# Kernel optimization log

Hardware: AMD Instinct MI355X
Metric: run time of the kernel (lower is better)

## Reference

```python
import jax, jax.numpy as jnp
import numpy as np

N, E, F_IN, H1, H2, C = 100000, 800000, 182, 128, 64, 2


def setup_inputs() -> dict:
    key = jax.random.key(0)
    ks = jax.random.split(key, 10)
    s = 0.05
    return {
        "x": jax.random.normal(ks[0], (N, F_IN), dtype=jnp.float32),
        "edge_index": jax.random.randint(ks[1], (2, E), 0, N, dtype=jnp.int32),
        "W1_l": jax.random.normal(ks[2], (H1, F_IN), dtype=jnp.float32) * s,
        "W1_r": jax.random.normal(ks[3], (H1, F_IN), dtype=jnp.float32) * s,
        "b1": jnp.zeros((H1,), dtype=jnp.float32),
        "W2_l": jax.random.normal(ks[4], (H2, H1), dtype=jnp.float32) * s,
        "W2_r": jax.random.normal(ks[5], (H2, H1), dtype=jnp.float32) * s,
        "b2": jnp.zeros((H2,), dtype=jnp.float32),
        "W_lin": jax.random.normal(ks[6], (C, H2), dtype=jnp.float32) * s,
        "b_lin": jnp.zeros((C,), dtype=jnp.float32),
    }


def _sage_conv(x, src, dst, Wl, Wr, b):
    # mean-aggregate neighbor messages x[src] onto dst, then two linears
    msg = x[src]                                            # [E, F]
    ssum = jax.ops.segment_sum(msg, dst, num_segments=N)    # [N, F]
    cnt = jax.ops.segment_sum(jnp.ones((src.shape[0], 1), x.dtype), dst, num_segments=N)
    mean = ssum / jnp.maximum(cnt, 1.0)                     # [N, F]
    return mean @ Wl.T + x @ Wr.T + b                       # [N, F_out]


def reference(x, edge_index, W1_l, W1_r, b1, W2_l, W2_r, b2, W_lin, b_lin):
    src, dst = edge_index[0], edge_index[1]
    h = jax.nn.relu(_sage_conv(x, src, dst, W1_l, W1_r, b1))   # dropout is identity in eval
    h = jax.nn.relu(_sage_conv(h, src, dst, W2_l, W2_r, b2))
    logits = h @ W_lin.T + b_lin
    return jax.nn.log_softmax(logits, axis=1)
```

## Files before the change

### kernel.cpp

```cpp
#include <hip/hip_runtime.h>
#include <hip/hip_bf16.h>
#include <math.h>

#define F_IN 182
#define H1   128
#define H2   64

typedef short bf16x8 __attribute__((ext_vector_type(8)));
typedef float f32x4 __attribute__((ext_vector_type(4)));

__device__ __forceinline__ float b2f(short s) {
    unsigned u = ((unsigned)(unsigned short)s) << 16;
    return __builtin_bit_cast(float, u);
}
__device__ __forceinline__ short f2b(float f) {
    return __builtin_bit_cast(short, __float2bfloat16(f));
}
__device__ __forceinline__ short2 f2x2(float2 f) {
    short2 r;
    r.x = f2b(f.x);
    r.y = f2b(f.y);
    return r;
}

#define GLOAD16(g, l) __builtin_amdgcn_global_load_lds( \
    (const __attribute__((address_space(1))) void*)(g), \
    (__attribute__((address_space(3))) void*)(l), 16, 0, 0)

__global__ __launch_bounds__(256) void prelude(
    int* __restrict__ cnt, int Nn, int zB,
    const float* __restrict__ W1l, const float* __restrict__ W1r, short* __restrict__ wc1,
    const float* __restrict__ W2l, const float* __restrict__ W2r, short* __restrict__ wc2)
{
    int b = blockIdx.x, tid = threadIdx.x;
    if (b < zB) {
        int i = (b * 256 + tid) * 4;
        if (i + 4 <= Nn) {
            int4 z = make_int4(0, 0, 0, 0);
            *(int4*)(cnt + i) = z;
        } else {
            for (int j = i; j < Nn; ++j) cnt[j] = 0;
        }
        return;
    }
    b -= zB;
    if (b < 192) {
        int idx = b * 256 + tid;
        int r = idx / 192, k = idx - r * 192;
        float v = 0.f;
        if (k < F_IN) v = (r < 128) ? W1l[r * F_IN + k] : W1r[(r - 128) * F_IN + k];
        wc1[idx] = f2b(v);
        return;
    }
    b -= 192;
    {
        int idx = b * 256 + tid;
        int r = idx >> 7, k = idx & 127;
        float v = (r < 64) ? W2l[r * 128 + k] : W2r[(r - 64) * 128 + k];
        wc2[idx] = f2b(v);
    }
}

__global__ __launch_bounds__(256) void scan_block(const int* __restrict__ in,
                                                  int* __restrict__ out,
                                                  int* __restrict__ bsums, int Nn) {
    __shared__ int s[256];
    int b = blockIdx.x, t = threadIdx.x;
    int base = b * 2048 + t * 8;
    int v[8]; int sum = 0;
#pragma unroll
    for (int i = 0; i < 8; ++i) { int idx = base + i; v[i] = (idx < Nn) ? in[idx] : 0; sum += v[i]; }
    s[t] = sum; __syncthreads();
    for (int off = 1; off < 256; off <<= 1) {
        int x = (t >= off) ? s[t - off] : 0; __syncthreads();
        s[t] += x; __syncthreads();
    }
    int excl = s[t] - sum;
    if (t == 255) bsums[b] = s[255];
    int run = excl;
#pragma unroll
    for (int i = 0; i < 8; ++i) { int idx = base + i; if (idx < Nn) out[idx] = run; run += v[i]; }
}

__global__ __launch_bounds__(256) void scan_add(int* __restrict__ offs,
                                                const int* __restrict__ bsums,
                                                int nb, int Nn) {
    __shared__ int sbs[64];
    int t = threadIdx.x;
    if (t < 64) {
        int v = (t < nb) ? bsums[t] : 0;
        int s = v;
#pragma unroll
        for (int off = 1; off < 64; off <<= 1) {
            int u = __shfl_up(s, off, 64);
            if (t >= off) s += u;
        }
        sbs[t] = s - v;
    }
    __syncthreads();
    int i = blockIdx.x * 256 + t;
    if (i < Nn) offs[i] += sbs[i >> 11];
}

__global__ __launch_bounds__(256) void csr_scatter(const int* __restrict__ srcv,
                                                   const int* __restrict__ dstv,
                                                   const int* __restrict__ rank,
                                                   const int* __restrict__ offs,
                                                   int* __restrict__ csr, int E) {
    int base = (blockIdx.x * 256 + threadIdx.x) * 8;
    if (base + 8 <= E) {
        int4 d0 = *(const int4*)(dstv + base);
        int4 d1 = *(const int4*)(dstv + base + 4);
        int4 s0 = *(const int4*)(srcv + base);
        int4 s1 = *(const int4*)(srcv + base + 4);
        int4 r0 = *(const int4*)(rank + base);
        int4 r1 = *(const int4*)(rank + base + 4);
        csr[offs[d0.x] + r0.x] = s0.x;
        csr[offs[d0.y] + r0.y] = s0.y;
        csr[offs[d0.z] + r0.z] = s0.z;
        csr[offs[d0.w] + r0.w] = s0.w;
        csr[offs[d1.x] + r1.x] = s1.x;
        csr[offs[d1.y] + r1.y] = s1.y;
        csr[offs[d1.z] + r1.z] = s1.z;
        csr[offs[d1.w] + r1.w] = s1.w;
    } else {
        for (int e = base; e < E; ++e) csr[offs[dstv[e]] + rank[e]] = srcv[e];
    }
}

template <int NC, int KK, int KREAL, bool DEG>
__global__ __launch_bounds__(512) void gemm_fused(
    const void* __restrict__ Ap, const short* __restrict__ Wcat,
    short* __restrict__ outL, short* __restrict__ outR, int M,
    const int* __restrict__ dstv, int* __restrict__ cnt, int* __restrict__ rank,
    int E, int degB)
{
    constexpr int BM = 128, BK = 64;
    constexpr int WN = NC / 4;
    constexpr int NJ = WN / 16;
    constexpr int CB = NC * 8 / 512;
    __shared__ __attribute__((aligned(16))) short sA[BM * BK];
    __shared__ __attribute__((aligned(16))) short sB[NC * BK];
    int tid = threadIdx.x;

    if (DEG && (int)blockIdx.x < degB) {
        int tstep = degB * 512 * 4;
        int gtid = (int)blockIdx.x * 512 + tid;
        for (int base = gtid * 4; base + 4 <= E; base += tstep) {
            int4 d = *(const int4*)(dstv + base);
            int4 rk;
            rk.x = atomicAdd(&cnt[d.x], 1);
            rk.y = atomicAdd(&cnt[d.y], 1);
            rk.z = atomicAdd(&cnt[d.z], 1);
            rk.w = atomicAdd(&cnt[d.w], 1);
            *(int4*)(rank + base) = rk;
        }
        if (gtid == 0) {
            for (int e = E & ~3; e < E; ++e) rank[e] = atomicAdd(&cnt[dstv[e]], 1);
        }
        return;
    }
    int bx = DEG ? ((int)blockIdx.x - degB) : (int)blockIdx.x;
    int wid = tid >> 6, lane = tid & 63;
    int wr = wid >> 2, wc = wid & 3;
    int row0 = bx * BM;
    f32x4 acc[4][NJ] = {};
#pragma unroll
    for (int ksi = 0; ksi < KK / BK; ++ksi) {
        const int k0 = ksi * BK;
        {
            const float* Af = (const float*)Ap;
#pragma unroll
            for (int it = 0; it < 2; ++it) {
                int i = it * 512 + tid;
                int r = i >> 3, oct = i & 7;
                int gr = row0 + r;
                int gk = k0 + oct * 8;
                bf16x8 v = {};
                if (gr < M) {
                    const float* p = Af + (size_t)gr * KREAL + gk;
                    if (k0 + BK <= KREAL) {
                        float2 f0 = *(const float2*)(p + 0);
                        float2 f1 = *(const float2*)(p + 2);
                        float2 f2 = *(const float2*)(p + 4);
                        float2 f3 = *(const float2*)(p + 6);
                        short2 p0 = f2x2(f0), p1 = f2x2(f1), p2 = f2x2(f2), p3 = f2x2(f3);
                        v[0] = p0.x; v[1] = p0.y; v[2] = p1.x; v[3] = p1.y;
                        v[4] = p2.x; v[5] = p2.y; v[6] = p3.x; v[7] = p3.y;
                    } else {
#pragma unroll
                        for (int j = 0; j < 4; ++j) {
                            if (gk + 2 * j + 2 <= KREAL) {
                                short2 pj = f2x2(*(const float2*)(p + 2 * j));
                                v[2 * j] = pj.x; v[2 * j + 1] = pj.y;
                            }
                        }
                    }
                }
                *(bf16x8*)((char*)sA + r * 128 + ((oct * 16) ^ ((r & 7) << 4))) = v;
            }
        }
#pragma unroll
        for (int c = 0; c < CB; ++c) {
            int idx = (wid * CB + c) * 64 + lane;
            int r = idx >> 3, cs = (idx & 7) * 16;
            const char* g = (const char*)Wcat + (size_t)r * (KK * 2) + k0 * 2 + (cs ^ ((r & 7) << 4));
            GLOAD16(g, (char*)sB + (size_t)(wid * CB + c) * 1024);
        }
        __syncthreads();
        int rl = lane & 15;
        int sw = (rl & 7) << 4;
#pragma unroll
        for (int ks = 0; ks < 2; ++ks) {
            int kb2 = ks * 64 + (lane >> 4) * 16;
            int cswz = kb2 ^ sw;
            bf16x8 af[4];
#pragma unroll
            for (int mi = 0; mi < 4; ++mi) {
                int row = wr * 64 + mi * 16 + rl;
                af[mi] = *(const bf16x8*)((const char*)sA + row * 128 + cswz);
            }
#pragma unroll
            for (int ni = 0; ni < NJ; ++ni) {
                int rowb = wc * WN + ni * 16 + rl;
                bf16x8 bfr = *(const bf16x8*)((const char*)sB + rowb * 128 + cswz);
#pragma unroll
                for (int mi = 0; mi < 4; ++mi)
                    acc[mi][ni] = __builtin_amdgcn_mfma_f32_16x16x32_bf16(af[mi], bfr, acc[mi][ni], 0, 0, 0);
            }
        }
        __syncthreads();
    }
    constexpr int HN = NC / 2;
#pragma unroll
    for (int mi = 0; mi < 4; ++mi) {
#pragma unroll
        for (int ni = 0; ni < NJ; ++ni) {
            int gc = wc * WN + ni * 16 + (lane & 15);
#pragma unroll
            for (int r = 0; r < 4; ++r) {
                int gr = row0 + wr * 64 + mi * 16 + (lane >> 4) * 4 + r;
                if (gr < M) {
                    short v = f2b(acc[mi][ni][r]);
                    if (gc < HN) outL[(size_t)gr * HN + gc] = v;
                    else         outR[(size_t)gr * HN + gc - HN] = v;
                }
            }
        }
    }
}

__global__ __launch_bounds__(512) void agg_gemm2(
    const int* __restrict__ offs, const int* __restrict__ degs, const int* __restrict__ csr,
    const short* __restrict__ y1l, const short* __restrict__ y1r,
    const float* __restrict__ b1, const short* __restrict__ wc2,
    short* __restrict__ outL, short* __restrict__ outR, int M)
{
    constexpr int BM = 128, NC = 128;
    constexpr int WN = NC / 4;
    constexpr int NJ = WN / 16;
    __shared__ __attribute__((aligned(16))) short sA[BM * 128];
    __shared__ __attribute__((aligned(16))) short sB[NC * 128];
    int tid = threadIdx.x;
    int wid = tid >> 6, lane = tid & 63;
    int wr = wid >> 2, wc = wid & 3;
    int row0 = (int)blockIdx.x * BM;

#pragma unroll
    for (int it = 0; it < 4; ++it) {
        int idx = (wid * 4 + it) * 64 + lane;
        int r = idx >> 4, c16 = (idx & 15) * 16;
        const char* g = (const char*)wc2 + (size_t)r * 256 + (c16 ^ ((r & 7) << 4));
        GLOAD16(g, (char*)sB + (size_t)(wid * 4 + it) * 1024);
    }

    int rlocal = tid >> 4;
    int l = tid & 15;
    const int co = l * 8;
#pragma unroll
    for (int rr = 0; rr < 4; ++rr) {
        int r = rr * 32 + rlocal;
        int gid = row0 + r;
        bf16x8 o = {};
        if (gid < M) {
            int start = offs[gid], deg = degs[gid];
            float a[8] = {};
            int t = 0;
            for (; t + 8 <= deg; t += 8) {
                int idx[8];
#pragma unroll
                for (int q = 0; q < 8; ++q) idx[q] = csr[start + t + q];
                bf16x8 vv[8];
#pragma unroll
                for (int q = 0; q < 8; ++q) vv[q] = *(const bf16x8*)(y1l + (size_t)idx[q] * H1 + co);
#pragma unroll
                for (int j = 0; j < 8; ++j) {
                    float s = 0.f;
#pragma unroll
                    for (int q = 0; q < 8; ++q) s += b2f(vv[q][j]);
                    a[j] += s;
                }
            }
            for (; t + 4 <= deg; t += 4) {
                int i0 = csr[start + t], i1 = csr[start + t + 1];
                int i2 = csr[start + t + 2], i3 = csr[start + t + 3];
                bf16x8 v0 = *(const bf16x8*)(y1l + (size_t)i0 * H1 + co);
                bf16x8 v1 = *(const bf16x8*)(y1l + (size_t)i1 * H1 + co);
                bf16x8 v2 = *(const bf16x8*)(y1l + (size_t)i2 * H1 + co);
                bf16x8 v3 = *(const bf16x8*)(y1l + (size_t)i3 * H1 + co);
#pragma unroll
                for (int j = 0; j < 8; ++j)
                    a[j] += b2f(v0[j]) + b2f(v1[j]) + b2f(v2[j]) + b2f(v3[j]);
            }
            for (; t < deg; ++t) {
                int s = csr[start + t];
                bf16x8 v = *(const bf16x8*)(y1l + (size_t)s * H1 + co);
#pragma unroll
                for (int j = 0; j < 8; ++j) a[j] += b2f(v[j]);
            }
            float inv = 1.f / fmaxf((float)deg, 1.f);
            bf16x8 rv = *(const bf16x8*)(y1r + (size_t)gid * H1 + co);
#pragma unroll
            for (int j = 0; j < 8; ++j)
                o[j] = f2b(fmaxf(a[j] * inv + b2f(rv[j]) + b1[co + j], 0.f));
        }
        *(bf16x8*)((char*)sA + r * 256 + ((co * 2) ^ ((r & 7) << 4))) = o;
    }
    __syncthreads();

    f32x4 acc[4][NJ] = {};
    int rl = lane & 15;
    int sw = (rl & 7) << 4;
#pragma unroll
    for (int ks = 0; ks < 4; ++ks) {
        int kcol = (ks * 4 + (lane >> 4)) * 16;
        int cswz = kcol ^ sw;
        bf16x8 af[4];
#pragma unroll
        for (int mi = 0; mi < 4; ++mi) {
            int row = wr * 64 + mi * 16 + rl;
            af[mi] = *(const bf16x8*)((const char*)sA + row * 256 + cswz);
        }
#pragma unroll
        for (int ni = 0; ni < NJ; ++ni) {
            int rowb = wc * WN + ni * 16 + rl;
            bf16x8 bfr = *(const bf16x8*)((const char*)sB + rowb * 256 + cswz);
#pragma unroll
            for (int mi = 0; mi < 4; ++mi)
                acc[mi][ni] = __builtin_amdgcn_mfma_f32_16x16x32_bf16(af[mi], bfr, acc[mi][ni], 0, 0, 0);
        }
    }
    constexpr int HN = NC / 2;
#pragma unroll
    for (int mi = 0; mi < 4; ++mi) {
#pragma unroll
        for (int ni = 0; ni < NJ; ++ni) {
            int gc = wc * WN + ni * 16 + (lane & 15);
#pragma unroll
            for (int r = 0; r < 4; ++r) {
                int gr = row0 + wr * 64 + mi * 16 + (lane >> 4) * 4 + r;
                if (gr < M) {
                    short v = f2b(acc[mi][ni][r]);
                    if (gc < HN) outL[(size_t)gr * HN + gc] = v;
                    else         outR[(size_t)gr * HN + gc - HN] = v;
                }
            }
        }
    }
}

__global__ __launch_bounds__(256) void agg_head2(const int* __restrict__ offs,
                                                 const int* __restrict__ degs,
                                                 const int* __restrict__ csr,
                                                 const short* __restrict__ yl,
                                                 const short* __restrict__ yr,
                                                 const float* __restrict__ bias,
                                                 const float* __restrict__ Wlin,
                                                 const float* __restrict__ blin,
                                                 float* __restrict__ out, int Nn) {
    int gid = blockIdx.x * 16 + (threadIdx.x >> 4);
    int l = threadIdx.x & 15;
    if (gid >= Nn) return;
    int start = offs[gid], deg = degs[gid];
    const int co = l * 4;
    float a[4] = {};
    int t = 0;
    for (; t + 8 <= deg; t += 8) {
        int idx[8];
#pragma unroll
        for (int q = 0; q < 8; ++q) idx[q] = csr[start + t + q];
        short4 vv[8];
#pragma unroll
        for (int q = 0; q < 8; ++q) vv[q] = *(const short4*)(yl + (size_t)idx[q] * H2 + co);
#pragma unroll
        for (int q = 0; q < 8; ++q) {
            a[0] += b2f(vv[q].x); a[1] += b2f(vv[q].y);
            a[2] += b2f(vv[q].z); a[3] += b2f(vv[q].w);
        }
    }
    for (; t + 4 <= deg; t += 4) {
        int i0 = csr[start + t], i1 = csr[start + t + 1];
        int i2 = csr[start + t + 2], i3 = csr[start + t + 3];
        short4 v0 = *(const short4*)(yl + (size_t)i0 * H2 + co);
        short4 v1 = *(const short4*)(yl + (size_t)i1 * H2 + co);
        short4 v2 = *(const short4*)(yl + (size_t)i2 * H2 + co);
        short4 v3 = *(const short4*)(yl + (size_t)i3 * H2 + co);
        a[0] += b2f(v0.x) + b2f(v1.x) + b2f(v2.x) + b2f(v3.x);
        a[1] += b2f(v0.y) + b2f(v1.y) + b2f(v2.y) + b2f(v3.y);
        a[2] += b2f(v0.z) + b2f(v1.z) + b2f(v2.z) + b2f(v3.z);
        a[3] += b2f(v0.w) + b2f(v1.w) + b2f(v2.w) + b2f(v3.w);
    }
    for (; t < deg; ++t) {
        int s = csr[start + t];
        short4 v = *(const short4*)(yl + (size_t)s * H2 + co);
        a[0] += b2f(v.x); a[1] += b2f(v.y); a[2] += b2f(v.z); a[3] += b2f(v.w);
    }
    float inv = 1.f / fmaxf((float)deg, 1.f);
    short4 rv = *(const short4*)(yr + (size_t)gid * H2 + co);
    float h0 = fmaxf(a[0] * inv + b2f(rv.x) + bias[co + 0], 0.f);
    float h1v = fmaxf(a[1] * inv + b2f(rv.y) + bias[co + 1], 0.f);
    float h2v = fmaxf(a[2] * inv + b2f(rv.z) + bias[co + 2], 0.f);
    float h3v = fmaxf(a[3] * inv + b2f(rv.w) + bias[co + 3], 0.f);
    float g0 = h0 * Wlin[co] + h1v * Wlin[co + 1] + h2v * Wlin[co + 2] + h3v * Wlin[co + 3];
    float g1 = h0 * Wlin[64 + co] + h1v * Wlin[64 + co + 1] + h2v * Wlin[64 + co + 2] + h3v * Wlin[64 + co + 3];
#pragma unroll
    for (int m = 8; m >= 1; m >>= 1) {
        g0 += __shfl_xor(g0, m, 16);
        g1 += __shfl_xor(g1, m, 16);
    }
    if (l == 0) {
        g0 += blin[0]; g1 += blin[1];
        float mx = fmaxf(g0, g1);
        float lse = mx + logf(expf(g0 - mx) + expf(g1 - mx));
        float2 r; r.x = g0 - lse; r.y = g1 - lse;
        ((float2*)out)[gid] = r;
    }
}

extern "C" void kernel_launch(void* const* d_in, const int* in_sizes, int n_in,
                              void* d_out, int out_size, void* d_ws, size_t ws_size,
                              hipStream_t stream) {
    const float* x    = (const float*)d_in[0];
    const int*   ei   = (const int*)d_in[1];
    const float* W1l  = (const float*)d_in[2];
    const float* W1r  = (const float*)d_in[3];
    const float* b1   = (const float*)d_in[4];
    const float* W2l  = (const float*)d_in[5];
    const float* W2r  = (const float*)d_in[6];
    const float* b2   = (const float*)d_in[7];
    const float* Wlin = (const float*)d_in[8];
    const float* blin = (const float*)d_in[9];
    float* outp = (float*)d_out;

    const int N = in_sizes[0] / F_IN;
    const int E = in_sizes[1] / 2;
    const int* srcv = ei;
    const int* dstv = ei + E;

    char* ws = (char*)d_ws;
    size_t o = 0;
    auto alloc = [&](size_t bytes) { size_t r = o; o += (bytes + 255) & ~(size_t)255; return r; };
    int* cnt_i  = (int*)(ws + alloc((size_t)N * 4));
    int* offs   = (int*)(ws + alloc((size_t)N * 4));
    int* bsums  = (int*)(ws + alloc(1024));
    int* rank   = (int*)(ws + alloc((size_t)E * 4));
    int* csr    = (int*)(ws + alloc((size_t)E * 4));
    short* wc1  = (short*)(ws + alloc((size_t)256 * 192 * 2));
    short* wc2  = (short*)(ws + alloc((size_t)128 * 128 * 2));
    short* y1l  = (short*)(ws + alloc((size_t)N * H1 * 2));
    short* y1r  = (short*)(ws + alloc((size_t)N * H1 * 2));
    short* y2l  = (short*)(ws + alloc((size_t)N * H2 * 2));
    short* y2r  = (short*)(ws + alloc((size_t)N * H2 * 2));

    const int zB   = (N + 1023) / 1024;
    const int degB = 64;
    const int nb   = (N + 2047) / 2048;
    const int nthr = (N + 255) / 256;
    const int gblk = (N + 127) / 128;
    const int e8   = (E + 2047) / 2048;
    const int a16  = (N + 15) / 16;

    prelude<<<zB + 192 + 64, 256, 0, stream>>>(cnt_i, N, zB, W1l, W1r, wc1, W2l, W2r, wc2);

    gemm_fused<256, 192, F_IN, true><<<degB + gblk, 512, 0, stream>>>(
        x, wc1, y1l, y1r, N, dstv, cnt_i, rank, E, degB);

    scan_block<<<nb, 256, 0, stream>>>(cnt_i, offs, bsums, N);
    scan_add<<<nthr, 256, 0, stream>>>(offs, bsums, nb, N);

    csr_scatter<<<e8, 256, 0, stream>>>(srcv, dstv, rank, offs, csr, E);

    agg_gemm2<<<gblk, 512, 0, stream>>>(offs, cnt_i, csr, y1l, y1r, b1, wc2, y2l, y2r, N);

    agg_head2<<<a16, 256, 0, stream>>>(offs, cnt_i, csr, y2l, y2r, b2, Wlin, blin, outp, N);
}
```

Baseline: 154.6 us.

## Fold block-sum scan offsets into consumers and read layer-2 weights from global

Replaces the full-array scan_add pass with a single-wave scan over the block sums. csr_scatter, agg_gemm2 and agg_head2 now add the block offset sbs[id>>11] themselves when they read a row start, which removes one pass over the 100k-entry offset array. Separately, agg_gemm2 no longer stages the 128x128 bf16 weight matrix in LDS and loads B fragments straight from global memory. This halves the kernel's shared memory, which may allow more blocks per CU, but those loads now sit inside the MFMA loop and depend on cache hits.

```diff
diff --git a/kernel.cpp b/kernel.cpp
--- a/kernel.cpp
+++ b/kernel.cpp
@@ -82,30 +82,23 @@
     for (int i = 0; i < 8; ++i) { int idx = base + i; if (idx < Nn) out[idx] = run; run += v[i]; }
 }
 
-__global__ __launch_bounds__(256) void scan_add(int* __restrict__ offs,
-                                                const int* __restrict__ bsums,
-                                                int nb, int Nn) {
-    __shared__ int sbs[64];
-    int t = threadIdx.x;
-    if (t < 64) {
-        int v = (t < nb) ? bsums[t] : 0;
-        int s = v;
-#pragma unroll
-        for (int off = 1; off < 64; off <<= 1) {
-            int u = __shfl_up(s, off, 64);
-            if (t >= off) s += u;
-        }
-        sbs[t] = s - v;
-    }
-    __syncthreads();
-    int i = blockIdx.x * 256 + t;
-    if (i < Nn) offs[i] += sbs[i >> 11];
+__global__ __launch_bounds__(64) void scan_bsums(int* bs, int nb) {
+    int l = threadIdx.x;
+    int v = (l < nb) ? bs[l] : 0;
+    int s = v;
+#pragma unroll
+    for (int off = 1; off < 64; off <<= 1) {
+        int t = __shfl_up(s, off, 64);
+        if (l >= off) s += t;
+    }
+    if (l < nb) bs[l] = s - v;
 }
 
 __global__ __launch_bounds__(256) void csr_scatter(const int* __restrict__ srcv,
                                                    const int* __restrict__ dstv,
                                                    const int* __restrict__ rank,
                                                    const int* __restrict__ offs,
+                                                   const int* __restrict__ sbs,
                                                    int* __restrict__ csr, int E) {
     int base = (blockIdx.x * 256 + threadIdx.x) * 8;
     if (base + 8 <= E) {
@@ -115,16 +108,17 @@
         int4 s1 = *(const int4*)(srcv + base + 4);
         int4 r0 = *(const int4*)(rank + base);
         int4 r1 = *(const int4*)(rank + base + 4);
-        csr[offs[d0.x] + r0.x] = s0.x;
-        csr[offs[d0.y] + r0.y] = s0.y;
-        csr[offs[d0.z] + r0.z] = s0.z;
-        csr[offs[d0.w] + r0.w] = s0.w;
-        csr[offs[d1.x] + r1.x] = s1.x;
-        csr[offs[d1.y] + r1.y] = s1.y;
-        csr[offs[d1.z] + r1.z] = s1.z;
-        csr[offs[d1.w] + r1.w] = s1.w;
+        csr[offs[d0.x] + sbs[d0.x >> 11] + r0.x] = s0.x;
+        csr[offs[d0.y] + sbs[d0.y >> 11] + r0.y] = s0.y;
+        csr[offs[d0.z] + sbs[d0.z >> 11] + r0.z] = s0.z;
+        csr[offs[d0.w] + sbs[d0.w >> 11] + r0.w] = s0.w;
+        csr[offs[d1.x] + sbs[d1.x >> 11] + r1.x] = s1.x;
+        csr[offs[d1.y] + sbs[d1.y >> 11] + r1.y] = s1.y;
+        csr[offs[d1.z] + sbs[d1.z >> 11] + r1.z] = s1.z;
+        csr[offs[d1.w] + sbs[d1.w >> 11] + r1.w] = s1.w;
     } else {
-        for (int e = base; e < E; ++e) csr[offs[dstv[e]] + rank[e]] = srcv[e];
+        for (int e = base; e < E; ++e)
+            csr[offs[dstv[e]] + sbs[dstv[e] >> 11] + rank[e]] = srcv[e];
     }
 }
 
@@ -251,7 +245,8 @@
 }
 
 __global__ __launch_bounds__(512) void agg_gemm2(
-    const int* __restrict__ offs, const int* __restrict__ degs, const int* __restrict__ csr,
+    const int* __restrict__ offs, const int* __restrict__ sbs,
+    const int* __restrict__ degs, const int* __restrict__ csr,
     const short* __restrict__ y1l, const short* __restrict__ y1r,
     const float* __restrict__ b1, const short* __restrict__ wc2,
     short* __restrict__ outL, short* __restrict__ outR, int M)
@@ -260,19 +255,10 @@
     constexpr int WN = NC / 4;
     constexpr int NJ = WN / 16;
     __shared__ __attribute__((aligned(16))) short sA[BM * 128];
-    __shared__ __attribute__((aligned(16))) short sB[NC * 128];
     int tid = threadIdx.x;
     int wid = tid >> 6, lane = tid & 63;
     int wr = wid >> 2, wc = wid & 3;
     int row0 = (int)blockIdx.x * BM;
-
-#pragma unroll
-    for (int it = 0; it < 4; ++it) {
-        int idx = (wid * 4 + it) * 64 + lane;
-        int r = idx >> 4, c16 = (idx & 15) * 16;
-        const char* g = (const char*)wc2 + (size_t)r * 256 + (c16 ^ ((r & 7) << 4));
-        GLOAD16(g, (char*)sB + (size_t)(wid * 4 + it) * 1024);
-    }
 
     int rlocal = tid >> 4;
     int l = tid & 15;
@@ -283,7 +269,8 @@
         int gid = row0 + r;
         bf16x8 o = {};
         if (gid < M) {
-            int start = offs[gid], deg = degs[gid];
+            int start = offs[gid] + sbs[gid >> 11];
+            int deg = degs[gid];
             float a[8] = {};
             int t = 0;
             for (; t + 8 <= deg; t += 8) {
@@ -344,7 +331,7 @@
 #pragma unroll
         for (int ni = 0; ni < NJ; ++ni) {
             int rowb = wc * WN + ni * 16 + rl;
-            bf16x8 bfr = *(const bf16x8*)((const char*)sB + rowb * 256 + cswz);
+            bf16x8 bfr = *(const bf16x8*)((const char*)wc2 + (size_t)rowb * 256 + kcol);
 #pragma unroll
             for (int mi = 0; mi < 4; ++mi)
                 acc[mi][ni] = __builtin_amdgcn_mfma_f32_16x16x32_bf16(af[mi], bfr, acc[mi][ni], 0, 0, 0);
@@ -370,6 +357,7 @@
 }
 
 __global__ __launch_bounds__(256) void agg_head2(const int* __restrict__ offs,
+                                                 const int* __restrict__ sbs,
                                                  const int* __restrict__ degs,
                                                  const int* __restrict__ csr,
                                                  const short* __restrict__ yl,
@@ -381,7 +369,8 @@
     int gid = blockIdx.x * 16 + (threadIdx.x >> 4);
     int l = threadIdx.x & 15;
     if (gid >= Nn) return;
-    int start = offs[gid], deg = degs[gid];
+    int start = offs[gid] + sbs[gid >> 11];
+    int deg = degs[gid];
     const int co = l * 4;
     float a[4] = {};
     int t = 0;
@@ -475,7 +464,6 @@
     const int zB   = (N + 1023) / 1024;
     const int degB = 64;
     const int nb   = (N + 2047) / 2048;
-    const int nthr = (N + 255) / 256;
     const int gblk = (N + 127) / 128;
     const int e8   = (E + 2047) / 2048;
     const int a16  = (N + 15) / 16;
@@ -486,11 +474,11 @@
         x, wc1, y1l, y1r, N, dstv, cnt_i, rank, E, degB);
 
     scan_block<<<nb, 256, 0, stream>>>(cnt_i, offs, bsums, N);
-    scan_add<<<nthr, 256, 0, stream>>>(offs, bsums, nb, N);
-
-    csr_scatter<<<e8, 256, 0, stream>>>(srcv, dstv, rank, offs, csr, E);
-
-    agg_gemm2<<<gblk, 512, 0, stream>>>(offs, cnt_i, csr, y1l, y1r, b1, wc2, y2l, y2r, N);
-
-    agg_head2<<<a16, 256, 0, stream>>>(offs, cnt_i, csr, y2l, y2r, b2, Wlin, blin, outp, N);
-}
+    scan_bsums<<<1, 64, 0, stream>>>(bsums, nb);
+
+    csr_scatter<<<e8, 256, 0, stream>>>(srcv, dstv, rank, offs, bsums, csr, E);
+
+    agg_gemm2<<<gblk, 512, 0, stream>>>(offs, bsums, cnt_i, csr, y1l, y1r, b1, wc2, y2l, y2r, N);
+
+    agg_head2<<<a16, 256, 0, stream>>>(offs, bsums, cnt_i, csr, y2l, y2r, b2, Wlin, blin, outp, N);
+}
```

New measurement: 158.0 us. +2.2%, slower.
